# Kernel tuning notes

Measured on AMD Instinct MI355X. Metric: run time of the kernel, lower is better.

Reference implementation:

```python
import itertools
import jax, jax.numpy as jnp
import numpy as np

INIT_STD = 0.1
N_PTS = 1_000_000
PLANE_RES = 512
OUT_DIM = 3
RANK = 8
FEAT_DIM = 32
FEAT_RES = 128


def grid_sample(grid, pts):
    """Equivalent of plenoxels grid_sample_wrapper / torch F.grid_sample.

    grid: [C, *spatial] (d spatial dims, d in {2,3})
    pts:  [N, d] in [-1, 1]; pts[:, k] indexes spatial dim d-1-k (torch x->W, y->H convention)
    bilinear/trilinear interpolation, align_corners=True, zeros padding.
    Returns [N, C].
    """
    spatial = grid.shape[1:]
    d = len(spatial)
    # sizes ordered per-pts-coordinate (reversed spatial order, torch convention)
    sizes_f = jnp.asarray([spatial[d - 1 - k] for k in range(d)], dtype=pts.dtype)
    sizes_i = jnp.asarray([spatial[d - 1 - k] for k in range(d)], dtype=jnp.int32)
    u = (pts + 1.0) * 0.5 * (sizes_f - 1.0)  # unnormalized coords, align_corners=True
    lo = jnp.floor(u)
    frac = u - lo  # [N, d]
    lo = lo.astype(jnp.int32)
    out = jnp.zeros((pts.shape[0], grid.shape[0]), dtype=pts.dtype)
    for corner in itertools.product((0, 1), repeat=d):  # 4 or 8 corners, fixed small loop
        ca = jnp.asarray(corner, dtype=jnp.int32)
        idx = lo + ca  # [N, d]
        valid = jnp.all((idx >= 0) & (idx < sizes_i), axis=-1)  # zeros padding outside
        w = jnp.prod(jnp.where(ca.astype(bool), frac, 1.0 - frac), axis=-1)
        w = w * valid.astype(pts.dtype)
        idx_c = jnp.clip(idx, 0, sizes_i - 1)
        # map pts-coord k back to spatial dim d-1-k for the gather
        vals = grid[(slice(None),) + tuple(idx_c[:, d - 1 - j] for j in range(d))]  # [C, N]
        out = out + w[:, None] * vals.T
    return out


def setup_inputs() -> dict:
    key = jax.random.key(0)
    k1, k2, k3, k4, k5 = jax.random.split(key, 5)
    pts = jax.random.uniform(k1, (N_PTS, 3), minval=-1.0, maxval=1.0, dtype=jnp.float32)
    C = OUT_DIM * RANK
    plane0 = INIT_STD * jax.random.normal(k2, (C, PLANE_RES, PLANE_RES), dtype=jnp.float32)
    plane1 = INIT_STD * jax.random.normal(k3, (C, PLANE_RES, PLANE_RES), dtype=jnp.float32)
    plane2 = INIT_STD * jax.random.normal(k4, (C, PLANE_RES, PLANE_RES), dtype=jnp.float32)
    features = INIT_STD * jax.random.normal(k5, (FEAT_DIM, FEAT_RES, FEAT_RES, FEAT_RES), dtype=jnp.float32)
    return {"pts": pts, "plane0": plane0, "plane1": plane1, "plane2": plane2, "features": features}


def reference(pts, plane0, plane1, plane2, features):
    """LowrankLearnableHash.compute_features: 3 plane bilinear gathers, elementwise
    multiply across planes, sum over rank, then trilinear lookup in feature volume."""
    n = pts.shape[0]
    combs = ((0, 1), (0, 2), (1, 2))  # itertools.combinations(range(3), 2)
    prod = None
    for plane, comb in zip((plane0, plane1, plane2), combs):
        s = grid_sample(plane, pts[:, jnp.asarray(comb)]).reshape(n, OUT_DIM, RANK)
        prod = s if prod is None else prod * s
    interp = prod.sum(axis=-1)  # [N, 3] coordinates into feature volume
    return grid_sample(features, interp)  # [N, FEAT_DIM]
```

## Files before the change

kernel.cpp:

```cpp
#include <hip/hip_runtime.h>

typedef float v4f __attribute__((ext_vector_type(4)));
typedef unsigned short u16;
typedef u16 u16x8 __attribute__((ext_vector_type(8)));

constexpr int PR  = 512;
constexpr int CP  = 24;
constexpr int FD  = 32;
constexpr int FR  = 128;
constexpr int PSZ = PR * PR;
constexpr int NBUCK = 32768;
constexpr int FW  = 16;
constexpr int FW0 = 56;
constexpr int RSTRIDE = 36;

__device__ inline u16 f2bf(float f) {
    unsigned u = __float_as_uint(f);
    return (u16)((u + 0x7fffu + ((u >> 16) & 1u)) >> 16);
}
__device__ inline float bf2f(u16 h) { return __uint_as_float((unsigned)h << 16); }

__global__ __launch_bounds__(256) void transpose_planes(
    const float* __restrict__ p0, const float* __restrict__ p1,
    const float* __restrict__ p2, u16* __restrict__ wsB)
{
    __shared__ float lds[CP][256];
    int b   = blockIdx.x;
    int p   = b >> 10;
    int rem = b & 1023;
    int y   = rem >> 1;
    int x0  = (rem & 1) << 8;
    const float* src = (p == 0) ? p0 : (p == 1) ? p1 : p2;
    int t = threadIdx.x;
    #pragma unroll
    for (int c = 0; c < CP; ++c)
        lds[c][t] = src[c * PSZ + y * PR + x0 + t];
    __syncthreads();
    int tex = y * PR + x0 + t;
    #pragma unroll
    for (int g = 0; g < 3; ++g) {
        u16x8 w;
        #pragma unroll
        for (int k = 0; k < 8; ++k) w[k] = f2bf(lds[g * 8 + k][t]);
        *(u16x8*)(wsB + ((size_t)(p * 3 + g) * PSZ + tex) * 8) = w;
    }
}

__global__ __launch_bounds__(256) void pack_feat(
    const float* __restrict__ feat, float* __restrict__ wsF)
{
    int t = blockIdx.x * 256 + threadIdx.x;
    int c = t & 31;
    int v = t >> 5;
    int x = v & 15, y = (v >> 4) & 15, z = v >> 8;
    wsF[(size_t)v * FD + c] =
        feat[(size_t)c * FR * FR * FR + (size_t)(z + FW0) * FR * FR
             + (y + FW0) * FR + (x + FW0)];
}

__global__ __launch_bounds__(256) void zero_hist(unsigned* __restrict__ hist)
{
    int t = blockIdx.x * 256 + threadIdx.x;
    v4f z = {0.f, 0.f, 0.f, 0.f};
    *(v4f*)(hist + t * 4) = z;
}

__device__ inline int cell5(float p) {
    int c = (int)floorf((p + 1.0f) * 16.0f);
    return min(max(c, 0), 31);
}
__device__ inline unsigned spread3(unsigned v) {
    return (v & 1u) | ((v & 2u) << 2) | ((v & 4u) << 4) | ((v & 8u) << 6) | ((v & 16u) << 8);
}
__device__ inline unsigned morton_key(float x, float y, float z) {
    return spread3((unsigned)cell5(x)) | (spread3((unsigned)cell5(y)) << 1)
         | (spread3((unsigned)cell5(z)) << 2);
}

__global__ __launch_bounds__(256) void bucket_hist(
    const float* __restrict__ pts, unsigned* __restrict__ hist, int n)
{
    int i = blockIdx.x * blockDim.x + threadIdx.x;
    if (i >= n) return;
    float x = pts[3 * i], y = pts[3 * i + 1], z = pts[3 * i + 2];
    atomicAdd(&hist[morton_key(x, y, z)], 1u);
}

__global__ __launch_bounds__(1024) void scan_offsets(
    const unsigned* __restrict__ hist, unsigned* __restrict__ cursor)
{
    __shared__ unsigned sums[1024];
    int t = threadIdx.x;
    const int base = t * (NBUCK / 1024);
    unsigned loc[NBUCK / 1024];
    unsigned s = 0;
    #pragma unroll
    for (int j = 0; j < NBUCK / 1024; ++j) { loc[j] = s; s += hist[base + j]; }
    sums[t] = s;
    __syncthreads();
    for (int off = 1; off < 1024; off <<= 1) {
        unsigned v = (t >= off) ? sums[t - off] : 0u;
        __syncthreads();
        sums[t] += v;
        __syncthreads();
    }
    unsigned blockbase = (t == 0) ? 0u : sums[t - 1];
    #pragma unroll
    for (int j = 0; j < NBUCK / 1024; ++j) cursor[base + j] = blockbase + loc[j];
}

__global__ __launch_bounds__(256) void scatter_pts(
    const float* __restrict__ pts, unsigned* __restrict__ cursor,
    v4f* __restrict__ sorted, int n)
{
    int i = blockIdx.x * blockDim.x + threadIdx.x;
    if (i >= n) return;
    float x = pts[3 * i], y = pts[3 * i + 1], z = pts[3 * i + 2];
    unsigned key = morton_key(x, y, z);
    unsigned pos = atomicAdd(&cursor[key], 1u);
    v4f v; v.x = x; v.y = y; v.z = z; v.w = __int_as_float(i);
    sorted[pos] = v;
}

template <int G>
__device__ inline float interp_group(const v4f pt, const u16* __restrict__ wsB)
{
    float cx[3] = {pt.x, pt.x, pt.y};
    float cy[3] = {pt.y, pt.z, pt.z};
    float pr[8] = {1.f, 1.f, 1.f, 1.f, 1.f, 1.f, 1.f, 1.f};
    #pragma unroll
    for (int p = 0; p < 3; ++p) {
        float ux = (cx[p] + 1.0f) * 0.5f * (float)(PR - 1);
        float uy = (cy[p] + 1.0f) * 0.5f * (float)(PR - 1);
        float lx = floorf(ux), ly = floorf(uy);
        float fx = ux - lx,   fy = uy - ly;
        int ix0 = (int)lx, iy0 = (int)ly;
        int ix1 = min(ix0 + 1, PR - 1);
        int iy1 = min(iy0 + 1, PR - 1);
        float wx0 = 1.f - fx, wx1 = fx;
        float wy0 = 1.f - fy, wy1 = fy;
        float w00 = wx0 * wy0, w01 = wx1 * wy0;
        float w10 = wx0 * wy1, w11 = wx1 * wy1;

        const u16* slab = wsB + (size_t)(p * 3 + G) * PSZ * 8;
        const u16x8 A = *(const u16x8*)(slab + (iy0 * PR + ix0) * 8);
        const u16x8 B = *(const u16x8*)(slab + (iy0 * PR + ix1) * 8);
        const u16x8 C = *(const u16x8*)(slab + (iy1 * PR + ix0) * 8);
        const u16x8 D = *(const u16x8*)(slab + (iy1 * PR + ix1) * 8);
        #pragma unroll
        for (int e = 0; e < 8; ++e) {
            float s = w00 * bf2f(A[e]) + w01 * bf2f(B[e])
                    + w10 * bf2f(C[e]) + w11 * bf2f(D[e]);
            pr[e] *= s;
        }
    }
    return ((pr[0] + pr[1]) + (pr[2] + pr[3]))
         + ((pr[4] + pr[5]) + (pr[6] + pr[7]));
}

template <int G>
__global__ __launch_bounds__(256, 8) void lrh_interp_g(
    const v4f* __restrict__ sorted, const u16* __restrict__ wsB,
    float* __restrict__ itp, int n)
{
    int nwg = gridDim.x;
    int q = nwg >> 3, r = nwg & 7;
    int xcd = blockIdx.x & 7, j = blockIdx.x >> 3;
    int wg = (xcd < r ? xcd * (q + 1) : r * (q + 1) + (xcd - r) * q) + j;
    int i = wg * 256 + threadIdx.x;
    if (i >= n) return;
    v4f pt = __builtin_nontemporal_load(&sorted[i]);
    float v = interp_group<G>(pt, wsB);
    __builtin_nontemporal_store(v, &itp[i]);
}

__global__ __launch_bounds__(256, 4) void lrh_g2_feat(
    const v4f* __restrict__ sorted, const u16* __restrict__ wsB,
    const float* __restrict__ itp0, const float* __restrict__ itp1,
    const float* __restrict__ wsF, const float* __restrict__ feat,
    float* __restrict__ out, int n)
{
    __shared__ float rows[256][RSTRIDE];
    __shared__ unsigned sord[256];

    int nwg = gridDim.x;
    int q = nwg >> 3, r0 = nwg & 7;
    int xcd = blockIdx.x & 7, jb = blockIdx.x >> 3;
    int wg = (xcd < r0 ? xcd * (q + 1) : r0 * (q + 1) + (xcd - r0) * q) + jb;
    int base = wg * 256;
    int t = threadIdx.x;
    int i = base + t;

    if (i < n) {
        v4f pt = __builtin_nontemporal_load(&sorted[i]);
        sord[t] = (unsigned)__float_as_int(pt.w);
        float v2 = interp_group<2>(pt, wsB);
        float ip[3];
        ip[0] = __builtin_nontemporal_load(&itp0[i]);
        ip[1] = __builtin_nontemporal_load(&itp1[i]);
        ip[2] = v2;

        float fr[3];
        int   j0[3];
        bool inw = true;
        #pragma unroll
        for (int k = 0; k < 3; ++k) {
            float uu = (ip[k] + 1.0f) * 0.5f * (float)(FR - 1);
            float lf = floorf(uu);
            fr[k] = uu - lf;
            j0[k] = (int)lf;
            inw = inw && (j0[k] >= FW0) && (j0[k] + 1 <= FW0 + FW - 1);
        }

        if (__builtin_expect(inw, 1)) {
            int lx = j0[0] - FW0, ly = j0[1] - FW0, lz = j0[2] - FW0;
            const float* cp = wsF + ((lz * FW + ly) * FW + lx) * FD;
            float wx1 = fr[0], wx0 = 1.f - fr[0];
            float wy1 = fr[1], wy0 = 1.f - fr[1];
            float wz1 = fr[2], wz0 = 1.f - fr[2];
            float wcn[8];
            int   ofs[8];
            #pragma unroll
            for (int m = 0; m < 8; ++m) {
                int bx = m & 1, by = (m >> 1) & 1, bz = m >> 2;
                wcn[m] = (bx ? wx1 : wx0) * (by ? wy1 : wy0) * (bz ? wz1 : wz0);
                ofs[m] = (bz * FW * FW + by * FW + bx) * FD;
            }
            #pragma unroll
            for (int cg = 0; cg < 8; ++cg) {
                v4f acc = {0.f, 0.f, 0.f, 0.f};
                #pragma unroll
                for (int m = 0; m < 8; ++m) {
                    v4f f = *(const v4f*)(cp + ofs[m] + cg * 4);
                    #pragma unroll
                    for (int c = 0; c < 4; ++c) acc[c] = fmaf(wcn[m], f[c], acc[c]);
                }
                *(v4f*)&rows[t][cg * 4] = acc;
            }
        } else {
            float v0[3], v1[3];
            int i0c[3], i1c[3];
            #pragma unroll
            for (int k = 0; k < 3; ++k) {
                int jj = j0[k];
                v0[k] = (jj   >= 0 && jj   < FR) ? 1.f : 0.f;
                v1[k] = (jj+1 >= 0 && jj+1 < FR) ? 1.f : 0.f;
                i0c[k] = min(max(jj,     0), FR - 1);
                i1c[k] = min(max(jj + 1, 0), FR - 1);
            }
            #pragma unroll
            for (int cg = 0; cg < 8; ++cg) {
                v4f acc = {0.f, 0.f, 0.f, 0.f};
                #pragma unroll
                for (int m = 0; m < 8; ++m) {
                    int bx = m & 1, by = (m >> 1) & 1, bz = m >> 2;
                    int xi = bx ? i1c[0] : i0c[0];
                    int yi = by ? i1c[1] : i0c[1];
                    int zi = bz ? i1c[2] : i0c[2];
                    float w = (bx ? fr[0] * v1[0] : (1.f - fr[0]) * v0[0])
                            * (by ? fr[1] * v1[1] : (1.f - fr[1]) * v0[1])
                            * (bz ? fr[2] * v1[2] : (1.f - fr[2]) * v0[2]);
                    int offc = zi * FR * FR + yi * FR + xi;
                    #pragma unroll
                    for (int c = 0; c < 4; ++c) {
                        const float* Fc = feat + (size_t)(cg * 4 + c) * (FR * FR * FR);
                        acc[c] = fmaf(w, Fc[offc], acc[c]);
                    }
                }
                *(v4f*)&rows[t][cg * 4] = acc;
            }
        }
    }
    __syncthreads();

    int e = t & 7;
    #pragma unroll
    for (int rb = 0; rb < 256; rb += 32) {
        int rr = rb + (t >> 3);
        if (base + rr < n) {
            unsigned orow = sord[rr];
            const float* lp = &rows[rr][e * 4];
            v4f v = {lp[0], lp[1], lp[2], lp[3]};
            *(v4f*)(out + (size_t)orow * FD + e * 4) = v;
        }
    }
}

extern "C" void kernel_launch(void* const* d_in, const int* in_sizes, int n_in,
                              void* d_out, int out_size, void* d_ws, size_t ws_size,
                              hipStream_t stream) {
    const float* pts  = (const float*)d_in[0];
    const float* p0   = (const float*)d_in[1];
    const float* p1   = (const float*)d_in[2];
    const float* p2   = (const float*)d_in[3];
    const float* feat = (const float*)d_in[4];
    float* out = (float*)d_out;
    int n = in_sizes[0] / 3;

    size_t off = 0;
    auto alloc = [&](size_t sz) { size_t o = off; off = (off + sz + 255) & ~(size_t)255; return o; };
    const size_t off_trans  = alloc((size_t)3 * PSZ * CP * sizeof(u16));
    const size_t off_sorted = alloc((size_t)n * sizeof(v4f));
    const size_t off_hist   = alloc(NBUCK * sizeof(unsigned));
    const size_t off_cursor = alloc(NBUCK * sizeof(unsigned));
    const size_t off_itp0   = alloc((size_t)n * sizeof(float));
    const size_t off_itp1   = alloc((size_t)n * sizeof(float));
    const size_t off_featw  = alloc((size_t)FW * FW * FW * FD * sizeof(float));

    char* ws = (char*)d_ws;
    u16*      wsB     = (u16*)(ws + off_trans);
    v4f*      sorted  = (v4f*)(ws + off_sorted);
    unsigned* hist    = (unsigned*)(ws + off_hist);
    unsigned* cursor  = (unsigned*)(ws + off_cursor);
    float*    itp0    = (float*)(ws + off_itp0);
    float*    itp1    = (float*)(ws + off_itp1);
    float*    wsF     = (float*)(ws + off_featw);

    int blocks = (n + 255) / 256;

    transpose_planes<<<3 * 1024, 256, 0, stream>>>(p0, p1, p2, wsB);
    pack_feat<<<(FW * FW * FW * FD) / 256, 256, 0, stream>>>(feat, wsF);
    zero_hist<<<NBUCK / (256 * 4), 256, 0, stream>>>(hist);
    bucket_hist<<<blocks, 256, 0, stream>>>(pts, hist, n);
    scan_offsets<<<1, 1024, 0, stream>>>(hist, cursor);
    scatter_pts<<<blocks, 256, 0, stream>>>(pts, cursor, sorted, n);
    lrh_interp_g<0><<<blocks, 256, 0, stream>>>(sorted, wsB, itp0, n);
    lrh_interp_g<1><<<blocks, 256, 0, stream>>>(sorted, wsB, itp1, n);
    lrh_g2_feat<<<blocks, 256, 0, stream>>>(sorted, wsB, itp0, itp1, wsF, feat, out, n);
}
```

Before: 295.0 us.

## Stage plane windows in LDS per Morton superbucket for group interpolation

```diff
diff --git a/kernel.cpp b/kernel.cpp
--- a/kernel.cpp
+++ b/kernel.cpp
@@ -10,6 +10,8 @@
 constexpr int FR  = 128;
 constexpr int PSZ = PR * PR;
 constexpr int NBUCK = 32768;
+constexpr int NSB  = 4096;
+constexpr int WW  = 34;
 constexpr int FW  = 16;
 constexpr int FW0 = 56;
 constexpr int RSTRIDE = 36;
@@ -72,6 +74,9 @@
 __device__ inline unsigned spread3(unsigned v) {
     return (v & 1u) | ((v & 2u) << 2) | ((v & 4u) << 4) | ((v & 8u) << 6) | ((v & 16u) << 8);
 }
+__device__ inline int compact3_4(unsigned v) {
+    return (v & 1u) | ((v >> 2) & 2u) | ((v >> 4) & 4u) | ((v >> 6) & 8u);
+}
 __device__ inline unsigned morton_key(float x, float y, float z) {
     return spread3((unsigned)cell5(x)) | (spread3((unsigned)cell5(y)) << 1)
          | (spread3((unsigned)cell5(z)) << 2);
@@ -87,7 +92,8 @@
 }
 
 __global__ __launch_bounds__(1024) void scan_offsets(
-    const unsigned* __restrict__ hist, unsigned* __restrict__ cursor)
+    const unsigned* __restrict__ hist, unsigned* __restrict__ cursor,
+    unsigned* __restrict__ sbbase, int n)
 {
     __shared__ unsigned sums[1024];
     int t = threadIdx.x;
@@ -106,7 +112,13 @@
     }
     unsigned blockbase = (t == 0) ? 0u : sums[t - 1];
     #pragma unroll
-    for (int j = 0; j < NBUCK / 1024; ++j) cursor[base + j] = blockbase + loc[j];
+    for (int j = 0; j < NBUCK / 1024; ++j) {
+        unsigned v = blockbase + loc[j];
+        int b = base + j;
+        cursor[b] = v;
+        if ((b & 7) == 0) sbbase[b >> 3] = v;
+    }
+    if (t == 0) sbbase[NSB] = (unsigned)n;
 }
 
 __global__ __launch_bounds__(256) void scatter_pts(
@@ -120,6 +132,73 @@
     unsigned pos = atomicAdd(&cursor[key], 1u);
     v4f v; v.x = x; v.y = y; v.z = z; v.w = __int_as_float(i);
     sorted[pos] = v;
+}
+
+template <int G>
+__global__ __launch_bounds__(256, 2) void lrh_interp_sb(
+    const v4f* __restrict__ sorted, const u16* __restrict__ wsB,
+    const unsigned* __restrict__ sbbase, float* __restrict__ itp)
+{
+    __shared__ u16x8 win[3][WW * WW];
+
+    int sb = (blockIdx.x & 7) * (NSB / 8) + (blockIdx.x >> 3);
+    int start = (int)sbbase[sb], end = (int)sbbase[sb + 1];
+    if (start >= end) return;
+
+    int t = threadIdx.x;
+    int X0 = compact3_4((unsigned)sb) << 1;
+    int Y0 = compact3_4((unsigned)sb >> 1) << 1;
+    int Z0 = compact3_4((unsigned)sb >> 2) << 1;
+    int bx = (X0 * (PR - 1)) >> 5;
+    int by = (Y0 * (PR - 1)) >> 5;
+    int bz = (Z0 * (PR - 1)) >> 5;
+    int wbu[3] = {bx, bx, by};
+    int wbv[3] = {by, bz, bz};
+
+    #pragma unroll
+    for (int p = 0; p < 3; ++p) {
+        const u16* slab = wsB + (size_t)(p * 3 + G) * PSZ * 8;
+        for (int k = t; k < WW * WW; k += 256) {
+            int row = k / WW, col = k - row * WW;
+            int gv = min(wbv[p] + row, PR - 1);
+            int gu = min(wbu[p] + col, PR - 1);
+            win[p][k] = *(const u16x8*)(slab + (gv * PR + gu) * 8);
+        }
+    }
+    __syncthreads();
+
+    for (int i = start + t; i < end; i += 256) {
+        v4f pt = sorted[i];
+        float cu[3] = {pt.x, pt.x, pt.y};
+        float cv[3] = {pt.y, pt.z, pt.z};
+        float pr[8] = {1.f, 1.f, 1.f, 1.f, 1.f, 1.f, 1.f, 1.f};
+        #pragma unroll
+        for (int p = 0; p < 3; ++p) {
+            float uu = (cu[p] + 1.0f) * 0.5f * (float)(PR - 1);
+            float vv = (cv[p] + 1.0f) * 0.5f * (float)(PR - 1);
+            float lu = floorf(uu), lv = floorf(vv);
+            float fu = uu - lu,   fv = vv - lv;
+            int lu0 = (int)lu - wbu[p];
+            int lv0 = (int)lv - wbv[p];
+            float wu0 = 1.f - fu, wu1 = fu;
+            float wv0 = 1.f - fv, wv1 = fv;
+            float w00 = wu0 * wv0, w01 = wu1 * wv0;
+            float w10 = wu0 * wv1, w11 = wu1 * wv1;
+            int c00 = lv0 * WW + lu0;
+            const u16x8 A = win[p][c00];
+            const u16x8 B = win[p][c00 + 1];
+            const u16x8 C = win[p][c00 + WW];
+            const u16x8 D = win[p][c00 + WW + 1];
+            #pragma unroll
+            for (int e = 0; e < 8; ++e) {
+                float s = w00 * bf2f(A[e]) + w01 * bf2f(B[e])
+                        + w10 * bf2f(C[e]) + w11 * bf2f(D[e]);
+                pr[e] *= s;
+            }
+        }
+        itp[i] = ((pr[0] + pr[1]) + (pr[2] + pr[3]))
+               + ((pr[4] + pr[5]) + (pr[6] + pr[7]));
+    }
 }
 
 template <int G>
@@ -156,22 +235,6 @@
     }
     return ((pr[0] + pr[1]) + (pr[2] + pr[3]))
          + ((pr[4] + pr[5]) + (pr[6] + pr[7]));
-}
-
-template <int G>
-__global__ __launch_bounds__(256, 8) void lrh_interp_g(
-    const v4f* __restrict__ sorted, const u16* __restrict__ wsB,
-    float* __restrict__ itp, int n)
-{
-    int nwg = gridDim.x;
-    int q = nwg >> 3, r = nwg & 7;
-    int xcd = blockIdx.x & 7, j = blockIdx.x >> 3;
-    int wg = (xcd < r ? xcd * (q + 1) : r * (q + 1) + (xcd - r) * q) + j;
-    int i = wg * 256 + threadIdx.x;
-    if (i >= n) return;
-    v4f pt = __builtin_nontemporal_load(&sorted[i]);
-    float v = interp_group<G>(pt, wsB);
-    __builtin_nontemporal_store(v, &itp[i]);
 }
 
 __global__ __launch_bounds__(256, 4) void lrh_g2_feat(
@@ -303,6 +366,7 @@
     const size_t off_sorted = alloc((size_t)n * sizeof(v4f));
     const size_t off_hist   = alloc(NBUCK * sizeof(unsigned));
     const size_t off_cursor = alloc(NBUCK * sizeof(unsigned));
+    const size_t off_sbb    = alloc((NSB + 1) * sizeof(unsigned));
     const size_t off_itp0   = alloc((size_t)n * sizeof(float));
     const size_t off_itp1   = alloc((size_t)n * sizeof(float));
     const size_t off_featw  = alloc((size_t)FW * FW * FW * FD * sizeof(float));
@@ -312,6 +376,7 @@
     v4f*      sorted  = (v4f*)(ws + off_sorted);
     unsigned* hist    = (unsigned*)(ws + off_hist);
     unsigned* cursor  = (unsigned*)(ws + off_cursor);
+    unsigned* sbbase  = (unsigned*)(ws + off_sbb);
     float*    itp0    = (float*)(ws + off_itp0);
     float*    itp1    = (float*)(ws + off_itp1);
     float*    wsF     = (float*)(ws + off_featw);
@@ -322,9 +387,9 @@
     pack_feat<<<(FW * FW * FW * FD) / 256, 256, 0, stream>>>(feat, wsF);
     zero_hist<<<NBUCK / (256 * 4), 256, 0, stream>>>(hist);
     bucket_hist<<<blocks, 256, 0, stream>>>(pts, hist, n);
-    scan_offsets<<<1, 1024, 0, stream>>>(hist, cursor);
+    scan_offsets<<<1, 1024, 0, stream>>>(hist, cursor, sbbase, n);
     scatter_pts<<<blocks, 256, 0, stream>>>(pts, cursor, sorted, n);
-    lrh_interp_g<0><<<blocks, 256, 0, stream>>>(sorted, wsB, itp0, n);
-    lrh_interp_g<1><<<blocks, 256, 0, stream>>>(sorted, wsB, itp1, n);
+    lrh_interp_sb<0><<<NSB, 256, 0, stream>>>(sorted, wsB, sbbase, itp0);
+    lrh_interp_sb<1><<<NSB, 256, 0, stream>>>(sorted, wsB, sbbase, itp1);
     lrh_g2_feat<<<blocks, 256, 0, stream>>>(sorted, wsB, itp0, itp1, wsF, feat, out, n);
 }
```

After: 315.0 us. 6.8% more time.
